# Performance work log

Hardware: AMD Instinct MI355X
Metric: run time of the kernel (lower is better)

Reference implementation:

```python
import jax, jax.numpy as jnp
import numpy as np


def setup_inputs() -> dict:
    key = jax.random.key(0)
    B, S, N, D = 4, 512, 8, 256
    ks = jax.random.split(key, 5)
    s = 0.02
    inp = {"x": jax.random.normal(ks[0], (B, S, N, D), jnp.float32)}
    for k, name in zip(ks[1:], ["Wq", "Wk", "Wv", "Wo"]):
        inp[name] = jax.random.normal(k, (D, D), jnp.float32) * s
    for name in ["bq", "bk", "bv", "bo"]:
        inp[name] = jnp.zeros((D,), jnp.float32)
    inp["gamma"] = jnp.ones((D,), jnp.float32)
    inp["beta"] = jnp.zeros((D,), jnp.float32)
    inp["num_heads"] = 8
    return inp


def reference(x, Wq, bq, Wk, bk, Wv, bv, Wo, bo, gamma, beta, num_heads):
    B, S, N, D = x.shape
    H = num_heads
    hd = D // H
    # sinusoidal positional encoding: even dims sin, odd dims cos
    pos = jnp.arange(S, dtype=jnp.float32)[:, None]                      # (S,1)
    div = jnp.exp(jnp.arange(0, D, 2, dtype=jnp.float32) * (-np.log(10000.0) / D))
    ang = pos * div                                                       # (S, D/2)
    pe = jnp.stack([jnp.sin(ang), jnp.cos(ang)], axis=-1).reshape(S, D)   # (S, D)
    x_pos = x + pe[None, :, None, :]                                      # (B,S,N,D)
    # fold sensors into batch: (B*N, S, D)
    xr = x_pos.transpose(0, 2, 1, 3).reshape(B * N, S, D)

    def proj(W, b):
        y = xr @ W.T + b                                                  # torch Linear
        return y.reshape(B * N, S, H, hd).transpose(0, 2, 1, 3)          # (BN,H,S,hd)

    Q, K, V = proj(Wq, bq), proj(Wk, bk), proj(Wv, bv)
    scores = jnp.einsum('bhqd,bhkd->bhqk', Q, K) / np.sqrt(hd)            # (BN,H,S,S)
    causal = jnp.tril(jnp.ones((S, S), dtype=bool))
    scores = jnp.where(causal[None, None], scores, jnp.float32(-1e9))
    attn = jax.nn.softmax(scores, axis=-1)                                # dropout = eval mode
    out = jnp.einsum('bhqk,bhkd->bhqd', attn, V)                          # (BN,H,S,hd)
    out = out.transpose(0, 2, 1, 3).reshape(B * N, S, D)
    out = out @ Wo.T + bo
    out = out.reshape(B, N, S, D).transpose(0, 2, 1, 3)                   # (B,S,N,D)
    y = out + x
    mu = jnp.mean(y, axis=-1, keepdims=True)
    var = jnp.var(y, axis=-1, keepdims=True)
    return (y - mu) / jnp.sqrt(var + 1e-5) * gamma + beta
```

## Files before the change

kernel.cpp:

```cpp
#include <hip/hip_runtime.h>
#include <hip/hip_bf16.h>
#include <math.h>

#define B_   4
#define S_   512
#define N_   8
#define D_   256
#define H_   8
#define HD_  32
#define BN_  32
#define MTOT (BN_ * S_)

typedef __attribute__((ext_vector_type(8))) short short8;
typedef __attribute__((ext_vector_type(4))) short short4v;
typedef __attribute__((ext_vector_type(4))) float floatx4;

#define QSCALE 0.25503468f

__device__ __forceinline__ float bf2f(short u) {
    union { unsigned u; float f; } c;
    c.u = ((unsigned)(unsigned short)u) << 16;
    return c.f;
}
__device__ __forceinline__ unsigned short f2bf(float f) {
    union { float f; unsigned u; } c; c.f = f;
    unsigned lsb = (c.u >> 16) & 1u;
    c.u += 0x7fffu + lsb;
    return (unsigned short)(c.u >> 16);
}
__device__ __forceinline__ unsigned short f2bf_ru(float f) {
    union { float f; unsigned u; } c; c.f = f;
    return (unsigned short)((c.u + 0x8000u) >> 16);
}
__device__ __forceinline__ float fexp2(float x) {
    float r; asm("v_exp_f32 %0, %1" : "=v"(r) : "v"(x)); return r;
}

__global__ __launch_bounds__(256) void prep_kernel(const float* __restrict__ x,
                                                   const float* __restrict__ Wq,
                                                   const float* __restrict__ Wk,
                                                   const float* __restrict__ Wv,
                                                   const float* __restrict__ Wo,
                                                   unsigned short* __restrict__ xpos,
                                                   unsigned short* __restrict__ wdst) {
    int bid = blockIdx.x;
    if (bid < 4096) {
        int idx4 = bid * 256 + threadIdx.x;
        int d0 = (idx4 << 2) & (D_ - 1);
        int s  = (idx4 >> 6) & (S_ - 1);
        int bn = idx4 >> 15;
        int b = bn >> 3, n = bn & 7;
        floatx4 xv = *(const floatx4*)(x + ((((size_t)b * S_ + s) * N_ + n) << 8) + d0);
        const float cfreq = -9.210340371976184f / 256.0f;
        float f0 = __expf((float)d0 * cfreq);
        float f1 = __expf((float)(d0 + 2) * cfreq);
        float a0 = (float)s * f0, a1 = (float)s * f1;
        short4v o;
        o[0] = (short)f2bf(xv[0] + __sinf(a0));
        o[1] = (short)f2bf(xv[1] + __cosf(a0));
        o[2] = (short)f2bf(xv[2] + __sinf(a1));
        o[3] = (short)f2bf(xv[3] + __cosf(a1));
        *(short4v*)(xpos + ((size_t)idx4 << 2)) = o;
    } else {
        int idx = (bid - 4096) * 256 + threadIdx.x;
        int which = idx >> 16, off = idx & 65535;
        const float* W = (which == 0) ? Wq : (which == 1) ? Wk : (which == 2) ? Wv : Wo;
        wdst[idx] = f2bf(W[off]);
    }
}

__global__ __launch_bounds__(256) void gemm_qkv_kernel(const unsigned short* __restrict__ A,
                                                       const unsigned short* __restrict__ W,
                                                       const float* __restrict__ bq,
                                                       const float* __restrict__ bk,
                                                       const float* __restrict__ bv,
                                                       unsigned short* __restrict__ Qb,
                                                       unsigned short* __restrict__ Kb,
                                                       unsigned short* __restrict__ Vt) {
    int wv = threadIdx.x >> 6, lane = threadIdx.x & 63;
    int col = lane & 15, quad = lane >> 4;
    int m_w = blockIdx.x * 128 + (wv >> 1) * 64;
    int n_w = blockIdx.y * 128 + (wv & 1) * 64;

    const short8* Ap = (const short8*)(A + (size_t)(m_w + col) * 256 + quad * 8);
    const short8* Bp = (const short8*)(W + (size_t)(n_w + col) * 256 + quad * 8);

    floatx4 acc[4][4] = {};
#pragma unroll
    for (int kk = 0; kk < 8; ++kk) {
        short8 a[4], b[4];
#pragma unroll
        for (int t = 0; t < 4; ++t) {
            a[t] = Ap[t * 512 + kk * 4];
            b[t] = Bp[t * 512 + kk * 4];
        }
#pragma unroll
        for (int mt = 0; mt < 4; ++mt)
#pragma unroll
            for (int nt = 0; nt < 4; ++nt)
                acc[mt][nt] = __builtin_amdgcn_mfma_f32_16x16x32_bf16(a[mt], b[nt], acc[mt][nt], 0, 0, 0);
    }

    int sel = blockIdx.y >> 1;
    const float* bias = (sel == 0) ? bq : (sel == 1) ? bk : bv;
#pragma unroll
    for (int nt = 0; nt < 4; ++nt) {
        int c = n_w + nt * 16 + col - sel * 256;
        float bv_ = bias[c];
#pragma unroll
        for (int mt = 0; mt < 4; ++mt) {
            int m0 = m_w + mt * 16 + quad * 4;
            if (sel == 2) {
                int bn = m0 >> 9, s0 = m0 & (S_ - 1);
                short4v pack;
#pragma unroll
                for (int r = 0; r < 4; ++r) pack[r] = (short)f2bf(acc[mt][nt][r] + bv_);
                *(short4v*)(Vt + (((size_t)((bn << 8) + c)) << 9) + s0) = pack;
            } else if (sel == 0) {
#pragma unroll
                for (int r = 0; r < 4; ++r)
                    Qb[((size_t)(m0 + r) << 8) | c] = f2bf((acc[mt][nt][r] + bv_) * QSCALE);
            } else {
#pragma unroll
                for (int r = 0; r < 4; ++r)
                    Kb[((size_t)(m0 + r) << 8) | c] = f2bf(acc[mt][nt][r] + bv_);
            }
        }
    }
}

__global__ __launch_bounds__(256) void gemm_o_kernel(const unsigned short* __restrict__ A,
                                                     const unsigned short* __restrict__ W,
                                                     const float* __restrict__ bo,
                                                     float* __restrict__ C) {
    int wv = threadIdx.x >> 6, lane = threadIdx.x & 63;
    int col = lane & 15, quad = lane >> 4;
    int m_w = blockIdx.x * 128 + (wv >> 1) * 64;
    int n_w = blockIdx.y * 128 + (wv & 1) * 64;

    const short8* Ap = (const short8*)(A + (size_t)(m_w + col) * 256 + quad * 8);
    const short8* Bp = (const short8*)(W + (size_t)(n_w + col) * 256 + quad * 8);

    floatx4 acc[4][4] = {};
#pragma unroll
    for (int kk = 0; kk < 8; ++kk) {
        short8 a[4], b[4];
#pragma unroll
        for (int t = 0; t < 4; ++t) {
            a[t] = Ap[t * 512 + kk * 4];
            b[t] = Bp[t * 512 + kk * 4];
        }
#pragma unroll
        for (int mt = 0; mt < 4; ++mt)
#pragma unroll
            for (int nt = 0; nt < 4; ++nt)
                acc[mt][nt] = __builtin_amdgcn_mfma_f32_16x16x32_bf16(a[mt], b[nt], acc[mt][nt], 0, 0, 0);
    }

#pragma unroll
    for (int nt = 0; nt < 4; ++nt) {
        int c = n_w + nt * 16 + col;
        float bv_ = bo[c];
#pragma unroll
        for (int mt = 0; mt < 4; ++mt) {
            int m0 = m_w + mt * 16 + quad * 4;
#pragma unroll
            for (int r = 0; r < 4; ++r)
                C[((size_t)(m0 + r) << 8) | c] = acc[mt][nt][r] + bv_;
        }
    }
}

#define PSTR 40
__global__ __launch_bounds__(256) void fattn_kernel(const unsigned short* __restrict__ Q,
                                                    const unsigned short* __restrict__ K,
                                                    const unsigned short* __restrict__ Vt,
                                                    unsigned short* __restrict__ O) {
    __shared__ unsigned short Plds[4][16 * PSTR];
    int wv = threadIdx.x >> 6, lane = threadIdx.x & 63;
    int col = lane & 15, quad = lane >> 4;
    int bnh  = blockIdx.x & 255;
    int qblk = blockIdx.x >> 8;
    int bn = bnh >> 3, h = bnh & 7;
    int q0 = qblk * 64 + wv * 16;

    unsigned short* P = &Plds[wv][0];

    short8 qfrag = *(const short8*)(Q + (((size_t)(bn * S_ + q0 + col)) << 8) + h * HD_ + quad * 8);
    const unsigned short* Kbase = K + (((size_t)(bn * S_)) << 8) + h * HD_ + quad * 8;
    const unsigned short* Vbase = Vt + (((size_t)(bnh * HD_)) << 9) + quad * 8;

    float l = 0.f;
    floatx4 o0 = {0.f, 0.f, 0.f, 0.f};
    floatx4 o1 = {0.f, 0.f, 0.f, 0.f};
    int lastk = q0 >> 5;

    for (int kt = 0; kt <= lastk; ++kt) {
        int k0 = kt * 32;
        short8 kf0 = *(const short8*)(Kbase + ((size_t)(k0 + col) << 8));
        short8 kf1 = *(const short8*)(Kbase + ((size_t)(k0 + 16 + col) << 8));
        floatx4 z = {0.f, 0.f, 0.f, 0.f};
        floatx4 st0 = __builtin_amdgcn_mfma_f32_16x16x32_bf16(kf0, qfrag, z, 0, 0, 0);
        floatx4 st1 = __builtin_amdgcn_mfma_f32_16x16x32_bf16(kf1, qfrag, z, 0, 0, 0);

        if (kt == lastk) {
            int qg = q0 + col;
#pragma unroll
            for (int r = 0; r < 4; ++r) {
                if (k0 + quad * 4 + r > qg)      st0[r] = -1e30f;
                if (k0 + 16 + quad * 4 + r > qg) st1[r] = -1e30f;
            }
        }

        float p[8]; float ts = 0.f;
#pragma unroll
        for (int r = 0; r < 4; ++r) {
            p[r]     = fexp2(st0[r]);
            p[4 + r] = fexp2(st1[r]);
            ts += p[r] + p[4 + r];
        }
        ts += __shfl_xor(ts, 16);
        ts += __shfl_xor(ts, 32);
        l += ts;

        short4v pk0, pk1;
#pragma unroll
        for (int r = 0; r < 4; ++r) {
            pk0[r] = (short)f2bf_ru(p[r]);
            pk1[r] = (short)f2bf_ru(p[4 + r]);
        }
        *(short4v*)&P[col * PSTR + quad * 4]      = pk0;
        *(short4v*)&P[col * PSTR + 16 + quad * 4] = pk1;
        asm volatile("s_waitcnt lgkmcnt(0)" ::: "memory");
        short8 pfrag = *(const short8*)&P[col * PSTR + quad * 8];

        short8 vf0 = *(const short8*)(Vbase + ((size_t)col << 9) + k0);
        short8 vf1 = *(const short8*)(Vbase + ((size_t)(16 + col) << 9) + k0);
        o0 = __builtin_amdgcn_mfma_f32_16x16x32_bf16(vf0, pfrag, o0, 0, 0, 0);
        o1 = __builtin_amdgcn_mfma_f32_16x16x32_bf16(vf1, pfrag, o1, 0, 0, 0);
    }

    float inv = 1.0f / l;
    unsigned short* Op = O + (((size_t)(bn * S_ + q0 + col)) << 8) + h * HD_;
    short4v s0v, s1v;
#pragma unroll
    for (int r = 0; r < 4; ++r) {
        s0v[r] = (short)f2bf(o0[r] * inv);
        s1v[r] = (short)f2bf(o1[r] * inv);
    }
    *(short4v*)(Op + quad * 4)      = s0v;
    *(short4v*)(Op + 16 + quad * 4) = s1v;
}

__global__ __launch_bounds__(64) void ln_kernel(const float* __restrict__ oproj,
                                                const float* __restrict__ x,
                                                const float* __restrict__ gamma,
                                                const float* __restrict__ beta,
                                                float* __restrict__ out) {
    int row = blockIdx.x;
    int bn = row >> 9, s = row & (S_ - 1);
    int b = bn >> 3, n = bn & 7;
    int lane = threadIdx.x;
    size_t obase = (((size_t)b * S_ + s) * N_ + n) << 8;

    floatx4 op = ((const floatx4*)(oproj + ((size_t)row << 8)))[lane];
    floatx4 xv = ((const floatx4*)(x + obase))[lane];
    float y[4];
    float sum = 0.f, ss = 0.f;
#pragma unroll
    for (int i = 0; i < 4; ++i) {
        y[i] = op[i] + xv[i];
        sum += y[i];
        ss  += y[i] * y[i];
    }
#pragma unroll
    for (int off = 32; off >= 1; off >>= 1) {
        sum += __shfl_xor(sum, off);
        ss  += __shfl_xor(ss, off);
    }
    float mu  = sum * (1.0f / 256.0f);
    float var = ss * (1.0f / 256.0f) - mu * mu;
    float rstd = rsqrtf(var + 1e-5f);

    int d0 = lane * 4;
    floatx4 o;
#pragma unroll
    for (int i = 0; i < 4; ++i)
        o[i] = (y[i] - mu) * rstd * gamma[d0 + i] + beta[d0 + i];
    ((floatx4*)(out + obase))[lane] = o;
}

extern "C" void kernel_launch(void* const* d_in, const int* in_sizes, int n_in,
                              void* d_out, int out_size, void* d_ws, size_t ws_size,
                              hipStream_t stream) {
    const float* x     = (const float*)d_in[0];
    const float* Wq    = (const float*)d_in[1];
    const float* Wk    = (const float*)d_in[2];
    const float* Wv    = (const float*)d_in[3];
    const float* Wo    = (const float*)d_in[4];
    const float* bq    = (const float*)d_in[5];
    const float* bk    = (const float*)d_in[6];
    const float* bv    = (const float*)d_in[7];
    const float* bo    = (const float*)d_in[8];
    const float* gamma = (const float*)d_in[9];
    const float* beta  = (const float*)d_in[10];

    char* w = (char*)d_ws;
    const size_t SZ = (size_t)MTOT * D_ * 2;
    unsigned short* xpos = (unsigned short*)(w);
    unsigned short* Qb   = (unsigned short*)(w + SZ);
    unsigned short* Kb   = (unsigned short*)(w + 2 * SZ);
    unsigned short* Vt   = (unsigned short*)(w + 3 * SZ);
    unsigned short* Ab   = (unsigned short*)(w + 4 * SZ);
    unsigned short* Wbf  = (unsigned short*)(w + 5 * SZ);
    float*          oproj = (float*)(w);

    prep_kernel<<<5120, 256, 0, stream>>>(x, Wq, Wk, Wv, Wo, xpos, Wbf);
    gemm_qkv_kernel<<<dim3(128, 6), 256, 0, stream>>>(xpos, Wbf, bq, bk, bv, Qb, Kb, Vt);
    fattn_kernel<<<2048, 256, 0, stream>>>(Qb, Kb, Vt, Ab);
    gemm_o_kernel<<<dim3(128, 2), 256, 0, stream>>>(Ab, Wbf + 3 * 65536, bo, oproj);
    ln_kernel<<<MTOT, 64, 0, stream>>>(oproj, x, gamma, beta, (float*)d_out);
}
```

Before: 173.3 us.

## Fuse output projection GEMM with residual add and LayerNorm epilogue

Merges the O-projection GEMM and the separate LayerNorm kernel into one kernel. Each block owns 64 full rows across all 256 columns, adds bias and the residual, reduces row statistics through shuffles and shared memory, then normalises and writes the output. This removes the fp32 intermediate write and re-read plus one launch. The risk is a different GEMM tiling (64x256 per block, 256 blocks) and strided per-element stores instead of vectorised ones.

```diff
diff --git a/kernel.cpp b/kernel.cpp
--- a/kernel.cpp
+++ b/kernel.cpp
@@ -129,48 +129,6 @@
     }
 }
 
-__global__ __launch_bounds__(256) void gemm_o_kernel(const unsigned short* __restrict__ A,
-                                                     const unsigned short* __restrict__ W,
-                                                     const float* __restrict__ bo,
-                                                     float* __restrict__ C) {
-    int wv = threadIdx.x >> 6, lane = threadIdx.x & 63;
-    int col = lane & 15, quad = lane >> 4;
-    int m_w = blockIdx.x * 128 + (wv >> 1) * 64;
-    int n_w = blockIdx.y * 128 + (wv & 1) * 64;
-
-    const short8* Ap = (const short8*)(A + (size_t)(m_w + col) * 256 + quad * 8);
-    const short8* Bp = (const short8*)(W + (size_t)(n_w + col) * 256 + quad * 8);
-
-    floatx4 acc[4][4] = {};
-#pragma unroll
-    for (int kk = 0; kk < 8; ++kk) {
-        short8 a[4], b[4];
-#pragma unroll
-        for (int t = 0; t < 4; ++t) {
-            a[t] = Ap[t * 512 + kk * 4];
-            b[t] = Bp[t * 512 + kk * 4];
-        }
-#pragma unroll
-        for (int mt = 0; mt < 4; ++mt)
-#pragma unroll
-            for (int nt = 0; nt < 4; ++nt)
-                acc[mt][nt] = __builtin_amdgcn_mfma_f32_16x16x32_bf16(a[mt], b[nt], acc[mt][nt], 0, 0, 0);
-    }
-
-#pragma unroll
-    for (int nt = 0; nt < 4; ++nt) {
-        int c = n_w + nt * 16 + col;
-        float bv_ = bo[c];
-#pragma unroll
-        for (int mt = 0; mt < 4; ++mt) {
-            int m0 = m_w + mt * 16 + quad * 4;
-#pragma unroll
-            for (int r = 0; r < 4; ++r)
-                C[((size_t)(m0 + r) << 8) | c] = acc[mt][nt][r] + bv_;
-        }
-    }
-}
-
 #define PSTR 40
 __global__ __launch_bounds__(256) void fattn_kernel(const unsigned short* __restrict__ Q,
                                                     const unsigned short* __restrict__ K,
@@ -252,42 +210,110 @@
     *(short4v*)(Op + 16 + quad * 4) = s1v;
 }
 
-__global__ __launch_bounds__(64) void ln_kernel(const float* __restrict__ oproj,
-                                                const float* __restrict__ x,
-                                                const float* __restrict__ gamma,
-                                                const float* __restrict__ beta,
-                                                float* __restrict__ out) {
-    int row = blockIdx.x;
-    int bn = row >> 9, s = row & (S_ - 1);
-    int b = bn >> 3, n = bn & 7;
-    int lane = threadIdx.x;
-    size_t obase = (((size_t)b * S_ + s) * N_ + n) << 8;
-
-    floatx4 op = ((const floatx4*)(oproj + ((size_t)row << 8)))[lane];
-    floatx4 xv = ((const floatx4*)(x + obase))[lane];
-    float y[4];
-    float sum = 0.f, ss = 0.f;
-#pragma unroll
-    for (int i = 0; i < 4; ++i) {
-        y[i] = op[i] + xv[i];
-        sum += y[i];
-        ss  += y[i] * y[i];
-    }
-#pragma unroll
-    for (int off = 32; off >= 1; off >>= 1) {
-        sum += __shfl_xor(sum, off);
-        ss  += __shfl_xor(ss, off);
-    }
-    float mu  = sum * (1.0f / 256.0f);
-    float var = ss * (1.0f / 256.0f) - mu * mu;
-    float rstd = rsqrtf(var + 1e-5f);
-
-    int d0 = lane * 4;
-    floatx4 o;
-#pragma unroll
-    for (int i = 0; i < 4; ++i)
-        o[i] = (y[i] - mu) * rstd * gamma[d0 + i] + beta[d0 + i];
-    ((floatx4*)(out + obase))[lane] = o;
+__global__ __launch_bounds__(256) void gemm_o_ln_kernel(const unsigned short* __restrict__ A,
+                                                        const unsigned short* __restrict__ W,
+                                                        const float* __restrict__ bo,
+                                                        const float* __restrict__ x,
+                                                        const float* __restrict__ gamma,
+                                                        const float* __restrict__ beta,
+                                                        float* __restrict__ out) {
+    __shared__ float lsum[4][64];
+    __shared__ float lss[4][64];
+    __shared__ float lmu[64];
+    __shared__ float lrs[64];
+
+    int wv = threadIdx.x >> 6, lane = threadIdx.x & 63;
+    int col = lane & 15, quad = lane >> 4;
+    int m_b = blockIdx.x * 64;
+    int n_w = wv * 64;
+
+    const short8* Ap = (const short8*)(A + (size_t)(m_b + col) * 256 + quad * 8);
+    const short8* Bp = (const short8*)(W + (size_t)(n_w + col) * 256 + quad * 8);
+
+    floatx4 acc[4][4] = {};
+#pragma unroll
+    for (int kk = 0; kk < 8; ++kk) {
+        short8 a[4], b[4];
+#pragma unroll
+        for (int t = 0; t < 4; ++t) {
+            a[t] = Ap[t * 512 + kk * 4];
+            b[t] = Bp[t * 512 + kk * 4];
+        }
+#pragma unroll
+        for (int mt = 0; mt < 4; ++mt)
+#pragma unroll
+            for (int nt = 0; nt < 4; ++nt)
+                acc[mt][nt] = __builtin_amdgcn_mfma_f32_16x16x32_bf16(a[mt], b[nt], acc[mt][nt], 0, 0, 0);
+    }
+
+    int bn = m_b >> 9, s0 = m_b & (S_ - 1);
+    int b_ = bn >> 3, n_ = bn & 7;
+    const float* xrow = x + ((((size_t)b_ * S_ + s0) * N_ + n_) << 8);
+    float* orow = out + ((((size_t)b_ * S_ + s0) * N_ + n_) << 8);
+
+    float psum[4][4] = {};
+    float pss[4][4]  = {};
+#pragma unroll
+    for (int nt = 0; nt < 4; ++nt) {
+        int c = n_w + nt * 16 + col;
+        float bv_ = bo[c];
+#pragma unroll
+        for (int mt = 0; mt < 4; ++mt) {
+            int sl = mt * 16 + quad * 4;
+#pragma unroll
+            for (int r = 0; r < 4; ++r) {
+                float y = acc[mt][nt][r] + bv_ + xrow[(size_t)(sl + r) * 2048 + c];
+                acc[mt][nt][r] = y;
+                psum[mt][r] += y;
+                pss[mt][r]  += y * y;
+            }
+        }
+    }
+#pragma unroll
+    for (int off = 8; off >= 1; off >>= 1) {
+#pragma unroll
+        for (int mt = 0; mt < 4; ++mt)
+#pragma unroll
+            for (int r = 0; r < 4; ++r) {
+                psum[mt][r] += __shfl_xor(psum[mt][r], off);
+                pss[mt][r]  += __shfl_xor(pss[mt][r], off);
+            }
+    }
+    if (col == 0) {
+#pragma unroll
+        for (int mt = 0; mt < 4; ++mt)
+#pragma unroll
+            for (int r = 0; r < 4; ++r) {
+                lsum[wv][mt * 16 + quad * 4 + r] = psum[mt][r];
+                lss[wv][mt * 16 + quad * 4 + r]  = pss[mt][r];
+            }
+    }
+    __syncthreads();
+    if (threadIdx.x < 64) {
+        int row = threadIdx.x;
+        float s  = lsum[0][row] + lsum[1][row] + lsum[2][row] + lsum[3][row];
+        float ss = lss[0][row] + lss[1][row] + lss[2][row] + lss[3][row];
+        float mu = s * (1.0f / 256.0f);
+        float var = ss * (1.0f / 256.0f) - mu * mu;
+        lmu[row] = mu;
+        lrs[row] = rsqrtf(var + 1e-5f);
+    }
+    __syncthreads();
+
+#pragma unroll
+    for (int nt = 0; nt < 4; ++nt) {
+        int c = n_w + nt * 16 + col;
+        float g  = gamma[c];
+        float be = beta[c];
+#pragma unroll
+        for (int mt = 0; mt < 4; ++mt) {
+            int sl = mt * 16 + quad * 4;
+#pragma unroll
+            for (int r = 0; r < 4; ++r)
+                orow[(size_t)(sl + r) * 2048 + c] =
+                    (acc[mt][nt][r] - lmu[sl + r]) * lrs[sl + r] * g + be;
+        }
+    }
 }
 
 extern "C" void kernel_launch(void* const* d_in, const int* in_sizes, int n_in,
@@ -313,11 +339,9 @@
     unsigned short* Vt   = (unsigned short*)(w + 3 * SZ);
     unsigned short* Ab   = (unsigned short*)(w + 4 * SZ);
     unsigned short* Wbf  = (unsigned short*)(w + 5 * SZ);
-    float*          oproj = (float*)(w);
 
     prep_kernel<<<5120, 256, 0, stream>>>(x, Wq, Wk, Wv, Wo, xpos, Wbf);
     gemm_qkv_kernel<<<dim3(128, 6), 256, 0, stream>>>(xpos, Wbf, bq, bk, bv, Qb, Kb, Vt);
     fattn_kernel<<<2048, 256, 0, stream>>>(Qb, Kb, Vt, Ab);
-    gemm_o_kernel<<<dim3(128, 2), 256, 0, stream>>>(Ab, Wbf + 3 * 65536, bo, oproj);
-    ln_kernel<<<MTOT, 64, 0, stream>>>(oproj, x, gamma, beta, (float*)d_out);
-}
+    gemm_o_ln_kernel<<<256, 256, 0, stream>>>(Ab, Wbf + 3 * 65536, bo, x, gamma, beta, (float*)d_out);
+}
```

Measured after the change: 167.7 us. -3.2%, faster.
